# Kernel tuning notes

Hardware: AMD Instinct MI355X
Metric: run time of the kernel (lower is better)

## Reference

```python
import jax, jax.numpy as jnp
import numpy as np

NUM_HEADS = 16

def _rope_tables(seq_len, head_dim, dtype):
    inv_freq = 1.0 / (10000.0 ** (jnp.arange(0, head_dim, 2, dtype=jnp.float32) / head_dim))
    t = jnp.arange(seq_len, dtype=jnp.float32)
    freqs = jnp.einsum('i,j->ij', t, inv_freq)          # [S, hd/2]
    emb = jnp.concatenate([freqs, freqs], axis=-1)      # [S, hd]
    return jnp.cos(emb).astype(dtype), jnp.sin(emb).astype(dtype)

def _rotate_half(x):
    x1, x2 = jnp.split(x, 2, axis=-1)
    return jnp.concatenate([-x2, x1], axis=-1)

def _apply_rope(x, cos, sin):
    # x: [B, H, S, hd]; cos/sin: [S, hd]
    return x * cos + _rotate_half(x) * sin

def setup_inputs() -> dict:
    key = jax.random.key(0)
    ks = jax.random.split(key, 9)
    S, B, E = 2048, 2, 1024
    sc_w = 1.0 / np.sqrt(E)
    inp = {
        'query': jax.random.normal(ks[0], (S, B, E), jnp.float32),
        'wq': jax.random.normal(ks[1], (E, E), jnp.float32) * sc_w,
        'bq': jax.random.normal(ks[2], (E,), jnp.float32) * 0.02,
        'wk': jax.random.normal(ks[3], (E, E), jnp.float32) * sc_w,
        'bk': jax.random.normal(ks[4], (E,), jnp.float32) * 0.02,
        'wv': jax.random.normal(ks[5], (E, E), jnp.float32) * sc_w,
        'bv': jax.random.normal(ks[6], (E,), jnp.float32) * 0.02,
        'wo': jax.random.normal(ks[7], (E, E), jnp.float32) * sc_w,
        'bo': jax.random.normal(ks[8], (E,), jnp.float32) * 0.02,
    }
    return inp

def reference(query, wq, bq, wk, bk, wv, bv, wo, bo):
    S, B, E = query.shape
    H = NUM_HEADS
    hd = E // H
    # QKV projections (torch Linear: x @ W^T + b). self_attention => k,v from query.
    q = jnp.einsum('sbe,fe->sbf', query, wq) + bq
    k = jnp.einsum('sbe,fe->sbf', query, wk) + bk
    v = jnp.einsum('sbe,fe->sbf', query, wv) + bv
    # [S, B, E] -> [B, H, S, hd]
    def to_bhsd(x):
        return x.reshape(S, B, H, hd).transpose(1, 2, 0, 3)
    q, k, v = to_bhsd(q), to_bhsd(k), to_bhsd(v)
    cos, sin = _rope_tables(S, hd, query.dtype)
    q = _apply_rope(q, cos, sin)
    k = _apply_rope(k, cos, sin)
    # scaled dot-product attention (no mask, no dropout)
    scale = 1.0 / jnp.sqrt(jnp.asarray(hd, query.dtype))
    scores = jnp.einsum('bhqd,bhkd->bhqk', q, k) * scale
    probs = jax.nn.softmax(scores, axis=-1)
    attn = jnp.einsum('bhqk,bhkd->bhqd', probs, v)
    # [B, H, S, hd] -> [S, B, E]
    attn = attn.transpose(2, 0, 1, 3).reshape(S, B, E)
    out = jnp.einsum('sbe,fe->sbf', attn, wo) + bo
    return out
```

## Files before the change

### kernel.cpp

```cpp
#include <hip/hip_runtime.h>
#include <stdint.h>

#define S_LEN 2048
#define BATCH 2
#define EMB   1024
#define NHEAD 16
#define HDIM  64

typedef __bf16 bf8   __attribute__((ext_vector_type(8)));
typedef float  f32x4 __attribute__((ext_vector_type(4)));
typedef float  f32x16 __attribute__((ext_vector_type(16)));

__device__ __forceinline__ unsigned short f2bf(float f) {
    unsigned u = __builtin_bit_cast(unsigned, f);
    u += 0x7fffu + ((u >> 16) & 1u);
    return (unsigned short)(u >> 16);
}
__device__ __forceinline__ float bf2f(unsigned short h) {
    unsigned u = ((unsigned)h) << 16;
    return __builtin_bit_cast(float, u);
}
__device__ __forceinline__ float fexp2(float x) { return __builtin_amdgcn_exp2f(x); }
__device__ __forceinline__ float f3max(float a, float b, float c) { return fmaxf(fmaxf(a, b), c); }

__device__ __forceinline__ void gl_lds16(const unsigned short* g, unsigned short* l) {
    __builtin_amdgcn_global_load_lds(
        (__attribute__((address_space(1))) void*)(void*)g,
        (__attribute__((address_space(3))) void*)(void*)l, 16, 0, 0);
}

__global__ void k_prep(const float* __restrict__ x,
                       const float* __restrict__ w0, const float* __restrict__ w1,
                       const float* __restrict__ w2, const float* __restrict__ w3,
                       float* __restrict__ cosT, float* __restrict__ sinT,
                       unsigned short* __restrict__ xb,
                       unsigned short* __restrict__ o0, unsigned short* __restrict__ o1,
                       unsigned short* __restrict__ o2, unsigned short* __restrict__ o3)
{
    int bid = blockIdx.x;
    if (bid < 512) {
        int idx = bid * 256 + threadIdx.x;
        int s = idx >> 6, d = idx & 63, j = d & 31;
        float inv = exp2f(-13.28771237954945f * ((float)j * (1.0f / 32.0f)));
        float ang = (float)s * inv;
        cosT[idx] = cosf(ang);
        sinT[idx] = sinf(ang);
    } else if (bid < 4608) {
        int id = (bid - 512) * 256 + threadIdx.x;
        int b = id >> 19, rem = id & 524287;
        int s = rem >> 8, e4 = (rem & 255) << 2;
        float4 v = *(const float4*)&x[((size_t)(s * BATCH + b)) * EMB + e4];
        ushort4 o;
        o.x = f2bf(v.x); o.y = f2bf(v.y); o.z = f2bf(v.z); o.w = f2bf(v.w);
        *(ushort4*)&xb[((size_t)(b * S_LEN + s)) * EMB + e4] = o;
    } else {
        int id = (bid - 4608) * 256 + threadIdx.x;
        int seg = id >> 18, r = id & 262143;
        const float* s = seg == 0 ? w0 : seg == 1 ? w1 : seg == 2 ? w2 : w3;
        unsigned short* o = seg == 0 ? o0 : seg == 1 ? o1 : seg == 2 ? o2 : o3;
        float4 v = *(const float4*)&s[(size_t)r * 4];
        ushort4 u;
        u.x = f2bf(v.x); u.y = f2bf(v.y); u.z = f2bf(v.z); u.w = f2bf(v.w);
        *(ushort4*)&o[(size_t)r * 4] = u;
    }
}

__global__ void __launch_bounds__(256) k_gemmQKV(
    const unsigned short* __restrict__ A,
    const unsigned short* __restrict__ Wq, const unsigned short* __restrict__ Wk,
    const unsigned short* __restrict__ Wv,
    const float* __restrict__ bqp, const float* __restrict__ bkp, const float* __restrict__ bvp,
    unsigned short* __restrict__ qout, unsigned short* __restrict__ kout,
    unsigned short* __restrict__ vout,
    const float* __restrict__ cosT, const float* __restrict__ sinT)
{
    __shared__ __align__(16) unsigned short As[128 * 32];
    __shared__ __align__(16) unsigned short Bs[128 * 32];
    const int z = blockIdx.z;
    const unsigned short* B = z == 0 ? Wq : z == 1 ? Wk : Wv;
    const float* bias = z == 0 ? bqp : z == 1 ? bkp : bvp;
    const int tid  = threadIdx.x;
    const int lane = tid & 63;
    const int wid  = tid >> 6;
    const int wm = wid >> 1, wn = wid & 1;
    const int l15 = lane & 15, lh = lane >> 4;
    const int tm0 = blockIdx.y * 128, tn0 = blockIdx.x * 128;
    const int K = 1024;

    f32x4 acc[4][4] = {};

    for (int k0 = 0; k0 < K; k0 += 32) {
        __syncthreads();
#pragma unroll
        for (int rnd = 0; rnd < 2; ++rnd) {
            int cbase = wid * 64 + rnd * 256;
            int c = cbase + lane;
            int row = c >> 2, co = (c & 3) * 8;
            gl_lds16(A + (size_t)(tm0 + row) * K + k0 + co, &As[cbase * 8]);
            gl_lds16(B + (size_t)(tn0 + row) * K + k0 + co, &Bs[cbase * 8]);
        }
        __syncthreads();
        bf8 a[4], b[4];
#pragma unroll
        for (int i = 0; i < 4; ++i) {
            a[i] = *(const bf8*)&As[(wm * 64 + i * 16 + l15) * 32 + lh * 8];
            b[i] = *(const bf8*)&Bs[(wn * 64 + i * 16 + l15) * 32 + lh * 8];
        }
#pragma unroll
        for (int i = 0; i < 4; ++i)
#pragma unroll
            for (int j = 0; j < 4; ++j)
                acc[i][j] = __builtin_amdgcn_mfma_f32_16x16x32_bf16(a[i], b[j], acc[i][j], 0, 0, 0);
    }

    if (z < 2) {
        unsigned short* C = z ? kout : qout;
        const float f = z ? 1.0f : 0.125f * 1.44269504089f;
#pragma unroll
        for (int i = 0; i < 4; ++i) {
            const int rowb = tm0 + wm * 64 + i * 16 + lh * 4;
#pragma unroll
            for (int j = 0; j < 2; ++j) {
                const int col = tn0 + wn * 64 + j * 16 + l15;
                const int d = j * 16 + l15;
#pragma unroll
                for (int r = 0; r < 4; ++r) {
                    int m = rowb + r;
                    int sq = m & (S_LEN - 1);
                    float x1 = acc[i][j][r]     + bias[col];
                    float x2 = acc[i][j + 2][r] + bias[col + 32];
                    float c  = cosT[sq * 64 + d] * f;
                    float sn = sinT[sq * 64 + d] * f;
                    C[(size_t)m * EMB + col]      = f2bf(x1 * c - x2 * sn);
                    C[(size_t)m * EMB + col + 32] = f2bf(x2 * c + x1 * sn);
                }
            }
        }
    } else {
#pragma unroll
        for (int i = 0; i < 4; ++i) {
            const int rowb = tm0 + wm * 64 + i * 16 + lh * 4;
#pragma unroll
            for (int j = 0; j < 4; ++j) {
                const int col = tn0 + wn * 64 + j * 16 + l15;
                float bv = bias[col];
#pragma unroll
                for (int r = 0; r < 4; ++r)
                    vout[(size_t)col * 4096 + rowb + r] = f2bf(acc[i][j][r] + bv);
            }
        }
    }
}

__global__ void __launch_bounds__(256) k_attn8(
    const unsigned short* __restrict__ qb,
    const unsigned short* __restrict__ kb,
    const unsigned short* __restrict__ vT,
    unsigned short* __restrict__ ob)
{
    __shared__ __align__(16) unsigned short Sm[24576];
    __shared__ float bl[4][32];
    const int tid = threadIdx.x, lane = tid & 63, wid = tid >> 6;
    const int l31 = lane & 31, hi = lane >> 5;
    const int bh = blockIdx.y;
    const int b = bh >> 4, h = bh & 15;
    const int q0 = blockIdx.x * 128 + wid * 32;

    const unsigned short* qrow = qb + ((size_t)(b * S_LEN + q0 + l31)) * EMB + h * HDIM + hi * 8;
    bf8 qf[4];
#pragma unroll
    for (int c = 0; c < 4; ++c) qf[c] = *(const bf8*)(qrow + c * 16);

    const int mz = l31 & 7;
    const int koA0 = l31 * 128 + (((0 * 2 + hi) ^ mz) << 4);
    const int koA1 = l31 * 128 + (((1 * 2 + hi) ^ mz) << 4);
    const int koA2 = l31 * 128 + (((2 * 2 + hi) ^ mz) << 4);
    const int koA3 = l31 * 128 + (((3 * 2 + hi) ^ mz) << 4);
    const char* ldsc = (const char*)Sm;

    const int srow = lane >> 3, sp = lane & 7;
    const int r0 = wid * 16 + srow,     p0s = sp ^ (r0 & 7);
    const int r1 = wid * 16 + 8 + srow, p1s = sp ^ (r1 & 7);
    const int kgo0 = (r0 * EMB + p0s * 8) * 2, kgo1 = (r1 * EMB + p1s * 8) * 2;
    const int vgo0 = (r0 * (S_LEN * BATCH) + p0s * 8) * 2, vgo1 = (r1 * (S_LEN * BATCH) + p1s * 8) * 2;

    const unsigned short* kS = kb + ((size_t)(b * S_LEN)) * EMB + h * HDIM;
    const unsigned short* vS = vT + ((size_t)h * HDIM) * (S_LEN * BATCH) + b * S_LEN;

#define STAGE8(DBUF) do { \
    gl_lds16((const unsigned short*)((const char*)kS + kgo0), Sm + (DBUF) * 4096 + wid * 1024); \
    gl_lds16((const unsigned short*)((const char*)vS + vgo0), Sm + 12288 + (DBUF) * 4096 + wid * 1024); \
    gl_lds16((const unsigned short*)((const char*)kS + kgo1), Sm + (DBUF) * 4096 + wid * 1024 + 512); \
    gl_lds16((const unsigned short*)((const char*)vS + vgo1), Sm + 12288 + (DBUF) * 4096 + wid * 1024 + 512); \
    kS += 64 * EMB; vS += 64; } while (0)

    auto pack2 = [](float lo, float hh) -> unsigned {
        unsigned short a  = __builtin_bit_cast(unsigned short, (__bf16)lo);
        unsigned short bb = __builtin_bit_cast(unsigned short, (__bf16)hh);
        return ((unsigned)bb << 16) | a;
    };

    float m_run = 0.f, l_run = 0.f;
    f32x16 oacc0 = {}, oacc1 = {};
    const f32x16 Z16 = {};

    STAGE8(0);
    STAGE8(1);

#define ABODY(BUF, DOSTG, LASTW) do { \
    if (LASTW) asm volatile("s_waitcnt vmcnt(0)" ::: "memory"); \
    else       asm volatile("s_waitcnt vmcnt(4)" ::: "memory"); \
    __builtin_amdgcn_s_barrier(); \
    if (DOSTG) STAGE8(((BUF) + 2) % 3); \
    bf8 ka0 = *(const bf8*)(ldsc + koA0 + (BUF) * 8192); \
    bf8 ka1 = *(const bf8*)(ldsc + koA1 + (BUF) * 8192); \
    bf8 ka2 = *(const bf8*)(ldsc + koA2 + (BUF) * 8192); \
    bf8 ka3 = *(const bf8*)(ldsc + koA3 + (BUF) * 8192); \
    bf8 kb0 = *(const bf8*)(ldsc + koA0 + (BUF) * 8192 + 4096); \
    bf8 kb1 = *(const bf8*)(ldsc + koA1 + (BUF) * 8192 + 4096); \
    bf8 kb2 = *(const bf8*)(ldsc + koA2 + (BUF) * 8192 + 4096); \
    bf8 kb3 = *(const bf8*)(ldsc + koA3 + (BUF) * 8192 + 4096); \
    __builtin_amdgcn_s_setprio(1); \
    f32x16 stA = __builtin_amdgcn_mfma_f32_32x32x16_bf16(ka0, qf[0], Z16, 0, 0, 0); \
    f32x16 stB = __builtin_amdgcn_mfma_f32_32x32x16_bf16(kb0, qf[0], Z16, 0, 0, 0); \
    stA = __builtin_amdgcn_mfma_f32_32x32x16_bf16(ka1, qf[1], stA, 0, 0, 0); \
    stB = __builtin_amdgcn_mfma_f32_32x32x16_bf16(kb1, qf[1], stB, 0, 0, 0); \
    stA = __builtin_amdgcn_mfma_f32_32x32x16_bf16(ka2, qf[2], stA, 0, 0, 0); \
    stB = __builtin_amdgcn_mfma_f32_32x32x16_bf16(kb2, qf[2], stB, 0, 0, 0); \
    stA = __builtin_amdgcn_mfma_f32_32x32x16_bf16(ka3, qf[3], stA, 0, 0, 0); \
    stB = __builtin_amdgcn_mfma_f32_32x32x16_bf16(kb3, qf[3], stB, 0, 0, 0); \
    __builtin_amdgcn_s_setprio(0); \
    float g0 = f3max(f3max(stA[0], stA[1], stA[2]),  f3max(stA[3], stA[4], stA[5]),  f3max(stA[6], stA[7], stA[8])); \
    float g1 = f3max(f3max(stA[9], stA[10], stA[11]), f3max(stA[12], stA[13], stA[14]), fmaxf(stA[15], stB[0])); \
    float g2 = f3max(f3max(stB[1], stB[2], stB[3]),  f3max(stB[4], stB[5], stB[6]),  f3max(stB[7], stB[8], stB[9])); \
    float g3 = f3max(f3max(stB[10], stB[11], stB[12]), f3max(stB[13], stB[14], stB[15]), fmaxf(g0, g1)); \
    float pmax = f3max(g2, g3, g0); \
    pmax = fmaxf(pmax, __shfl_xor(pmax, 32)); \
    if (!__all(pmax - m_run <= 11.54f)) { \
        float mnew = fmaxf(m_run, pmax); \
        float corr = fexp2(m_run - mnew); \
        l_run *= corr; m_run = mnew; \
        if (hi == 0) bl[wid][l31] = corr; \
        asm volatile("s_waitcnt lgkmcnt(0)" ::: "memory"); \
        _Pragma("unroll") for (int r = 0; r < 16; ++r) { \
            float c2 = bl[wid][(r & 3) + 8 * (r >> 2) + 4 * hi]; \
            oacc0[r] *= c2; oacc1[r] *= c2; } \
    } \
    float pA[16], pB[16]; \
    _Pragma("unroll") for (int r = 0; r < 16; ++r) pA[r] = fexp2(stA[r] - m_run); \
    _Pragma("unroll") for (int r = 0; r < 16; ++r) pB[r] = fexp2(stB[r] - m_run); \
    float sA = (((pA[0] + pA[1]) + (pA[2] + pA[3])) + ((pA[4] + pA[5]) + (pA[6] + pA[7]))) \
             + (((pA[8] + pA[9]) + (pA[10] + pA[11])) + ((pA[12] + pA[13]) + (pA[14] + pA[15]))); \
    float sB = (((pB[0] + pB[1]) + (pB[2] + pB[3])) + ((pB[4] + pB[5]) + (pB[6] + pB[7]))) \
             + (((pB[8] + pB[9]) + (pB[10] + pB[11])) + ((pB[12] + pB[13]) + (pB[14] + pB[15]))); \
    float psum = sA + sB; \
    psum += __shfl_xor(psum, 32); \
    l_run += psum; \
    unsigned a0w = pack2(pA[0], pA[1]),  a1w = pack2(pA[2], pA[3]); \
    unsigned a2w = pack2(pA[4], pA[5]),  a3w = pack2(pA[6], pA[7]); \
    unsigned a4w = pack2(pA[8], pA[9]),  a5w = pack2(pA[10], pA[11]); \
    unsigned a6w = pack2(pA[12], pA[13]), a7w = pack2(pA[14], pA[15]); \
    unsigned rA_ = (unsigned)__shfl_xor((int)(hi ? a0w : a2w), 32); \
    unsigned rB_ = (unsigned)__shfl_xor((int)(hi ? a1w : a3w), 32); \
    unsigned rC_ = (unsigned)__shfl_xor((int)(hi ? a4w : a6w), 32); \
    unsigned rD_ = (unsigned)__shfl_xor((int)(hi ? a5w : a7w), 32); \
    uint4 uA0 = hi ? uint4{rA_, rB_, a2w, a3w} : uint4{a0w, a1w, rA_, rB_}; \
    uint4 uA1 = hi ? uint4{rC_, rD_, a6w, a7w} : uint4{a4w, a5w, rC_, rD_}; \
    bf8 pf0A = __builtin_bit_cast(bf8, uA0); \
    bf8 pf1A = __builtin_bit_cast(bf8, uA1); \
    unsigned b0w = pack2(pB[0], pB[1]),  b1w = pack2(pB[2], pB[3]); \
    unsigned b2w = pack2(pB[4], pB[5]),  b3w = pack2(pB[6], pB[7]); \
    unsigned b4w = pack2(pB[8], pB[9]),  b5w = pack2(pB[10], pB[11]); \
    unsigned b6w = pack2(pB[12], pB[13]), b7w = pack2(pB[14], pB[15]); \
    unsigned rE_ = (unsigned)__shfl_xor((int)(hi ? b0w : b2w), 32); \
    unsigned rF_ = (unsigned)__shfl_xor((int)(hi ? b1w : b3w), 32); \
    unsigned rG_ = (unsigned)__shfl_xor((int)(hi ? b4w : b6w), 32); \
    unsigned rH_ = (unsigned)__shfl_xor((int)(hi ? b5w : b7w), 32); \
    uint4 uB0 = hi ? uint4{rE_, rF_, b2w, b3w} : uint4{b0w, b1w, rE_, rF_}; \
    uint4 uB1 = hi ? uint4{rG_, rH_, b6w, b7w} : uint4{b4w, b5w, rG_, rH_}; \
    bf8 pf0B = __builtin_bit_cast(bf8, uB0); \
    bf8 pf1B = __builtin_bit_cast(bf8, uB1); \
    bf8 va0 = *(const bf8*)(ldsc + koA0 + 24576 + (BUF) * 8192); \
    bf8 va1 = *(const bf8*)(ldsc + koA1 + 24576 + (BUF) * 8192); \
    bf8 va2 = *(const bf8*)(ldsc + koA2 + 24576 + (BUF) * 8192); \
    bf8 va3 = *(const bf8*)(ldsc + koA3 + 24576 + (BUF) * 8192); \
    bf8 vb0 = *(const bf8*)(ldsc + koA0 + 24576 + (BUF) * 8192 + 4096); \
    bf8 vb1 = *(const bf8*)(ldsc + koA1 + 24576 + (BUF) * 8192 + 4096); \
    bf8 vb2 = *(const bf8*)(ldsc + koA2 + 24576 + (BUF) * 8192 + 4096); \
    bf8 vb3 = *(const bf8*)(ldsc + koA3 + 24576 + (BUF) * 8192 + 4096); \
    __builtin_amdgcn_s_setprio(1); \
    oacc0 = __builtin_amdgcn_mfma_f32_32x32x16_bf16(pf0A, va0, oacc0, 0, 0, 0); \
    oacc1 = __builtin_amdgcn_mfma_f32_32x32x16_bf16(pf0A, vb0, oacc1, 0, 0, 0); \
    oacc0 = __builtin_amdgcn_mfma_f32_32x32x16_bf16(pf1A, va1, oacc0, 0, 0, 0); \
    oacc1 = __builtin_amdgcn_mfma_f32_32x32x16_bf16(pf1A, vb1, oacc1, 0, 0, 0); \
    oacc0 = __builtin_amdgcn_mfma_f32_32x32x16_bf16(pf0B, va2, oacc0, 0, 0, 0); \
    oacc1 = __builtin_amdgcn_mfma_f32_32x32x16_bf16(pf0B, vb2, oacc1, 0, 0, 0); \
    oacc0 = __builtin_amdgcn_mfma_f32_32x32x16_bf16(pf1B, va3, oacc0, 0, 0, 0); \
    oacc1 = __builtin_amdgcn_mfma_f32_32x32x16_bf16(pf1B, vb3, oacc1, 0, 0, 0); \
    __builtin_amdgcn_s_setprio(0); \
} while (0)

    for (int t3 = 0; t3 < 10; ++t3) {
        ABODY(0, true, false);
        ABODY(1, true, false);
        ABODY(2, true, false);
    }
    ABODY(0, false, false);
    ABODY(1, false, true);

#undef ABODY
#undef STAGE8

    if (hi == 0) bl[wid][l31] = l_run;
    asm volatile("s_waitcnt lgkmcnt(0)" ::: "memory");
#pragma unroll
    for (int r = 0; r < 16; ++r) {
        int q = (r & 3) + 8 * (r >> 2) + 4 * hi;
        float linv = 1.0f / bl[wid][q];
        size_t base = ((size_t)(b * S_LEN + q0 + q)) * EMB + h * HDIM + l31;
        ob[base]      = f2bf(oacc0[r] * linv);
        ob[base + 32] = f2bf(oacc1[r] * linv);
    }
}

template<int EPI, typename OutT>
__global__ void __launch_bounds__(256) k_gemm(
    const unsigned short* __restrict__ A,
    const unsigned short* __restrict__ B,
    const float* __restrict__ bias,
    OutT* __restrict__ C,
    int M, int N, int K)
{
    __shared__ __align__(16) unsigned short As[128 * 32];
    __shared__ __align__(16) unsigned short Bs[128 * 32];
    const int tid  = threadIdx.x;
    const int lane = tid & 63;
    const int wid  = tid >> 6;
    const int wm = wid >> 1, wn = wid & 1;
    const int l15 = lane & 15, lh = lane >> 4;
    const int tm0 = blockIdx.y * 128, tn0 = blockIdx.x * 128;

    f32x4 acc[4][4] = {};

    for (int k0 = 0; k0 < K; k0 += 32) {
        __syncthreads();
#pragma unroll
        for (int rnd = 0; rnd < 2; ++rnd) {
            int cbase = wid * 64 + rnd * 256;
            int c = cbase + lane;
            int row = c >> 2, co = (c & 3) * 8;
            gl_lds16(A + (size_t)(tm0 + row) * K + k0 + co, &As[cbase * 8]);
            gl_lds16(B + (size_t)(tn0 + row) * K + k0 + co, &Bs[cbase * 8]);
        }
        __syncthreads();
        bf8 a[4], b[4];
#pragma unroll
        for (int i = 0; i < 4; ++i) {
            a[i] = *(const bf8*)&As[(wm * 64 + i * 16 + l15) * 32 + lh * 8];
            b[i] = *(const bf8*)&Bs[(wn * 64 + i * 16 + l15) * 32 + lh * 8];
        }
#pragma unroll
        for (int i = 0; i < 4; ++i)
#pragma unroll
            for (int j = 0; j < 4; ++j)
                acc[i][j] = __builtin_amdgcn_mfma_f32_16x16x32_bf16(a[i], b[j], acc[i][j], 0, 0, 0);
    }

#pragma unroll
    for (int i = 0; i < 4; ++i) {
        const int rowb = tm0 + wm * 64 + i * 16 + lh * 4;
#pragma unroll
        for (int j = 0; j < 4; ++j) {
            const int col = tn0 + wn * 64 + j * 16 + l15;
#pragma unroll
            for (int r = 0; r < 4; ++r) {
                float v = acc[i][j][r];
                int row = rowb + r;
                if (EPI == 0) {
                    v += bias[col];
                    C[(size_t)row * N + col] = (OutT)f2bf(v);
                } else {
                    v += bias[col];
                    int bb = row >> 11, ss = row & 2047;
                    ((float*)C)[(size_t)(ss * BATCH + bb) * N + col] = v;
                }
            }
        }
    }
}

extern "C" void kernel_launch(void* const* d_in, const int* in_sizes, int n_in,
                              void* d_out, int out_size, void* d_ws, size_t ws_size,
                              hipStream_t stream)
{
    (void)in_sizes; (void)n_in; (void)out_size; (void)ws_size;
    const float* query = (const float*)d_in[0];
    const float* wq = (const float*)d_in[1];
    const float* bq = (const float*)d_in[2];
    const float* wk = (const float*)d_in[3];
    const float* bk = (const float*)d_in[4];
    const float* wv = (const float*)d_in[5];
    const float* bv = (const float*)d_in[6];
    const float* wo = (const float*)d_in[7];
    const float* bo = (const float*)d_in[8];

    char* ws = (char*)d_ws;
    float*          cosT = (float*)(ws + 0);
    float*          sinT = (float*)(ws + (512 << 10));
    unsigned short* xb   = (unsigned short*)(ws + (1  << 20));
    unsigned short* wqb  = (unsigned short*)(ws + (9  << 20));
    unsigned short* wkb  = (unsigned short*)(ws + (11 << 20));
    unsigned short* wvb  = (unsigned short*)(ws + (13 << 20));
    unsigned short* wob  = (unsigned short*)(ws + (15 << 20));
    unsigned short* qb   = (unsigned short*)(ws + (17 << 20));
    unsigned short* ob   = qb;
    unsigned short* kb   = (unsigned short*)(ws + (25 << 20));
    unsigned short* vT   = (unsigned short*)(ws + (33 << 20));

    k_prep<<<8704, 256, 0, stream>>>(query, wq, wk, wv, wo,
                                     cosT, sinT, xb, wqb, wkb, wvb, wob);

    dim3 gq(EMB / 128, (S_LEN * BATCH) / 128, 3);
    k_gemmQKV<<<gq, 256, 0, stream>>>(xb, wqb, wkb, wvb, bq, bk, bv,
                                      qb, kb, vT, cosT, sinT);

    dim3 g3(S_LEN / 128, BATCH * NHEAD);
    k_attn8<<<g3, 256, 0, stream>>>(qb, kb, vT, ob);

    dim3 g1(EMB / 128, (S_LEN * BATCH) / 128);
    k_gemm<1, float><<<g1, 256, 0, stream>>>(ob, wob, bo, (float*)d_out, 4096, 1024, 1024);
}
```

Before: 153.8 us.

## Process two 32-row query tiles per wave in attention kernel

The attention kernel now uses 2 waves (128 threads) per block instead of 4, and each wave handles 64 query rows as two 32-row tiles. The K and V fragments read from LDS are reused by both tiles, and each wave stages twice as many K/V rows. This halves LDS fragment reads per query row and lets one tile's softmax interleave with the other tile's MFMAs. The cost is higher register pressure from doubled accumulators and Q fragments, and fewer waves per block, which may reduce occupancy and latency hiding.

```diff
diff --git a/kernel.cpp b/kernel.cpp
--- a/kernel.cpp
+++ b/kernel.cpp
@@ -152,24 +152,28 @@
     }
 }
 
-__global__ void __launch_bounds__(256) k_attn8(
+__global__ void __launch_bounds__(128) k_attn9(
     const unsigned short* __restrict__ qb,
     const unsigned short* __restrict__ kb,
     const unsigned short* __restrict__ vT,
     unsigned short* __restrict__ ob)
 {
     __shared__ __align__(16) unsigned short Sm[24576];
-    __shared__ float bl[4][32];
+    __shared__ float bl[2][2][32];
     const int tid = threadIdx.x, lane = tid & 63, wid = tid >> 6;
     const int l31 = lane & 31, hi = lane >> 5;
     const int bh = blockIdx.y;
     const int b = bh >> 4, h = bh & 15;
-    const int q0 = blockIdx.x * 128 + wid * 32;
-
-    const unsigned short* qrow = qb + ((size_t)(b * S_LEN + q0 + l31)) * EMB + h * HDIM + hi * 8;
-    bf8 qf[4];
-#pragma unroll
-    for (int c = 0; c < 4; ++c) qf[c] = *(const bf8*)(qrow + c * 16);
+    const int q0 = blockIdx.x * 128 + wid * 64;
+
+    const unsigned short* qrowA = qb + ((size_t)(b * S_LEN + q0 + l31)) * EMB + h * HDIM + hi * 8;
+    const unsigned short* qrowB = qrowA + (size_t)32 * EMB;
+    bf8 qfA[4], qfB[4];
+#pragma unroll
+    for (int c = 0; c < 4; ++c) {
+        qfA[c] = *(const bf8*)(qrowA + c * 16);
+        qfB[c] = *(const bf8*)(qrowB + c * 16);
+    }
 
     const int mz = l31 & 7;
     const int koA0 = l31 * 128 + (((0 * 2 + hi) ^ mz) << 4);
@@ -179,19 +183,23 @@
     const char* ldsc = (const char*)Sm;
 
     const int srow = lane >> 3, sp = lane & 7;
-    const int r0 = wid * 16 + srow,     p0s = sp ^ (r0 & 7);
-    const int r1 = wid * 16 + 8 + srow, p1s = sp ^ (r1 & 7);
-    const int kgo0 = (r0 * EMB + p0s * 8) * 2, kgo1 = (r1 * EMB + p1s * 8) * 2;
-    const int vgo0 = (r0 * (S_LEN * BATCH) + p0s * 8) * 2, vgo1 = (r1 * (S_LEN * BATCH) + p1s * 8) * 2;
+    int kgo[4], vgo[4];
+#pragma unroll
+    for (int i = 0; i < 4; ++i) {
+        int ri = wid * 32 + i * 8 + srow;
+        int ps = sp ^ (ri & 7);
+        kgo[i] = (ri * EMB + ps * 8) * 2;
+        vgo[i] = (ri * (S_LEN * BATCH) + ps * 8) * 2;
+    }
 
     const unsigned short* kS = kb + ((size_t)(b * S_LEN)) * EMB + h * HDIM;
     const unsigned short* vS = vT + ((size_t)h * HDIM) * (S_LEN * BATCH) + b * S_LEN;
 
-#define STAGE8(DBUF) do { \
-    gl_lds16((const unsigned short*)((const char*)kS + kgo0), Sm + (DBUF) * 4096 + wid * 1024); \
-    gl_lds16((const unsigned short*)((const char*)vS + vgo0), Sm + 12288 + (DBUF) * 4096 + wid * 1024); \
-    gl_lds16((const unsigned short*)((const char*)kS + kgo1), Sm + (DBUF) * 4096 + wid * 1024 + 512); \
-    gl_lds16((const unsigned short*)((const char*)vS + vgo1), Sm + 12288 + (DBUF) * 4096 + wid * 1024 + 512); \
+#define STAGE9(DBUF) do { \
+    _Pragma("unroll") for (int i = 0; i < 4; ++i) { \
+        gl_lds16((const unsigned short*)((const char*)kS + kgo[i]), Sm + (DBUF) * 4096 + wid * 2048 + i * 512); \
+        gl_lds16((const unsigned short*)((const char*)vS + vgo[i]), Sm + 12288 + (DBUF) * 4096 + wid * 2048 + i * 512); \
+    } \
     kS += 64 * EMB; vS += 64; } while (0)
 
     auto pack2 = [](float lo, float hh) -> unsigned {
@@ -200,18 +208,77 @@
         return ((unsigned)bb << 16) | a;
     };
 
-    float m_run = 0.f, l_run = 0.f;
-    f32x16 oacc0 = {}, oacc1 = {};
+    float m_runA = 0.f, l_runA = 0.f, m_runB = 0.f, l_runB = 0.f;
+    f32x16 oA0 = {}, oA1 = {}, oB0 = {}, oB1 = {};
     const f32x16 Z16 = {};
 
-    STAGE8(0);
-    STAGE8(1);
+    auto softmax_tile = [&](f32x16& stA, f32x16& stB, float& m_run, float& l_run,
+                            int ti, f32x16& o0, f32x16& o1,
+                            bf8& pf0A, bf8& pf1A, bf8& pf0B, bf8& pf1B) __attribute__((always_inline)) {
+        float g0 = f3max(f3max(stA[0], stA[1], stA[2]),  f3max(stA[3], stA[4], stA[5]),  f3max(stA[6], stA[7], stA[8]));
+        float g1 = f3max(f3max(stA[9], stA[10], stA[11]), f3max(stA[12], stA[13], stA[14]), fmaxf(stA[15], stB[0]));
+        float g2 = f3max(f3max(stB[1], stB[2], stB[3]),  f3max(stB[4], stB[5], stB[6]),  f3max(stB[7], stB[8], stB[9]));
+        float g3 = f3max(f3max(stB[10], stB[11], stB[12]), f3max(stB[13], stB[14], stB[15]), fmaxf(g0, g1));
+        float pmax = f3max(g2, g3, g0);
+        pmax = fmaxf(pmax, __shfl_xor(pmax, 32));
+        if (!__all(pmax - m_run <= 11.54f)) {
+            float mnew = fmaxf(m_run, pmax);
+            float corr = fexp2(m_run - mnew);
+            l_run *= corr; m_run = mnew;
+            if (hi == 0) bl[wid][ti][l31] = corr;
+            asm volatile("s_waitcnt lgkmcnt(0)" ::: "memory");
+#pragma unroll
+            for (int r = 0; r < 16; ++r) {
+                float c2 = bl[wid][ti][(r & 3) + 8 * (r >> 2) + 4 * hi];
+                o0[r] *= c2; o1[r] *= c2;
+            }
+        }
+        float pA[16], pB[16];
+#pragma unroll
+        for (int r = 0; r < 16; ++r) pA[r] = fexp2(stA[r] - m_run);
+#pragma unroll
+        for (int r = 0; r < 16; ++r) pB[r] = fexp2(stB[r] - m_run);
+        float sA = (((pA[0] + pA[1]) + (pA[2] + pA[3])) + ((pA[4] + pA[5]) + (pA[6] + pA[7])))
+                 + (((pA[8] + pA[9]) + (pA[10] + pA[11])) + ((pA[12] + pA[13]) + (pA[14] + pA[15])));
+        float sB = (((pB[0] + pB[1]) + (pB[2] + pB[3])) + ((pB[4] + pB[5]) + (pB[6] + pB[7])))
+                 + (((pB[8] + pB[9]) + (pB[10] + pB[11])) + ((pB[12] + pB[13]) + (pB[14] + pB[15])));
+        float psum = sA + sB;
+        psum += __shfl_xor(psum, 32);
+        l_run += psum;
+        unsigned a0w = pack2(pA[0], pA[1]),  a1w = pack2(pA[2], pA[3]);
+        unsigned a2w = pack2(pA[4], pA[5]),  a3w = pack2(pA[6], pA[7]);
+        unsigned a4w = pack2(pA[8], pA[9]),  a5w = pack2(pA[10], pA[11]);
+        unsigned a6w = pack2(pA[12], pA[13]), a7w = pack2(pA[14], pA[15]);
+        unsigned rA_ = (unsigned)__shfl_xor((int)(hi ? a0w : a2w), 32);
+        unsigned rB_ = (unsigned)__shfl_xor((int)(hi ? a1w : a3w), 32);
+        unsigned rC_ = (unsigned)__shfl_xor((int)(hi ? a4w : a6w), 32);
+        unsigned rD_ = (unsigned)__shfl_xor((int)(hi ? a5w : a7w), 32);
+        uint4 u0 = hi ? uint4{rA_, rB_, a2w, a3w} : uint4{a0w, a1w, rA_, rB_};
+        uint4 u1 = hi ? uint4{rC_, rD_, a6w, a7w} : uint4{a4w, a5w, rC_, rD_};
+        pf0A = __builtin_bit_cast(bf8, u0);
+        pf1A = __builtin_bit_cast(bf8, u1);
+        unsigned b0w = pack2(pB[0], pB[1]),  b1w = pack2(pB[2], pB[3]);
+        unsigned b2w = pack2(pB[4], pB[5]),  b3w = pack2(pB[6], pB[7]);
+        unsigned b4w = pack2(pB[8], pB[9]),  b5w = pack2(pB[10], pB[11]);
+        unsigned b6w = pack2(pB[12], pB[13]), b7w = pack2(pB[14], pB[15]);
+        unsigned rE_ = (unsigned)__shfl_xor((int)(hi ? b0w : b2w), 32);
+        unsigned rF_ = (unsigned)__shfl_xor((int)(hi ? b1w : b3w), 32);
+        unsigned rG_ = (unsigned)__shfl_xor((int)(hi ? b4w : b6w), 32);
+        unsigned rH_ = (unsigned)__shfl_xor((int)(hi ? b5w : b7w), 32);
+        uint4 w0 = hi ? uint4{rE_, rF_, b2w, b3w} : uint4{b0w, b1w, rE_, rF_};
+        uint4 w1 = hi ? uint4{rG_, rH_, b6w, b7w} : uint4{b4w, b5w, rG_, rH_};
+        pf0B = __builtin_bit_cast(bf8, w0);
+        pf1B = __builtin_bit_cast(bf8, w1);
+    };
+
+    STAGE9(0);
+    STAGE9(1);
 
 #define ABODY(BUF, DOSTG, LASTW) do { \
     if (LASTW) asm volatile("s_waitcnt vmcnt(0)" ::: "memory"); \
-    else       asm volatile("s_waitcnt vmcnt(4)" ::: "memory"); \
+    else       asm volatile("s_waitcnt vmcnt(8)" ::: "memory"); \
     __builtin_amdgcn_s_barrier(); \
-    if (DOSTG) STAGE8(((BUF) + 2) % 3); \
+    if (DOSTG) STAGE9(((BUF) + 2) % 3); \
     bf8 ka0 = *(const bf8*)(ldsc + koA0 + (BUF) * 8192); \
     bf8 ka1 = *(const bf8*)(ldsc + koA1 + (BUF) * 8192); \
     bf8 ka2 = *(const bf8*)(ldsc + koA2 + (BUF) * 8192); \
@@ -221,65 +288,29 @@
     bf8 kb2 = *(const bf8*)(ldsc + koA2 + (BUF) * 8192 + 4096); \
     bf8 kb3 = *(const bf8*)(ldsc + koA3 + (BUF) * 8192 + 4096); \
     __builtin_amdgcn_s_setprio(1); \
-    f32x16 stA = __builtin_amdgcn_mfma_f32_32x32x16_bf16(ka0, qf[0], Z16, 0, 0, 0); \
-    f32x16 stB = __builtin_amdgcn_mfma_f32_32x32x16_bf16(kb0, qf[0], Z16, 0, 0, 0); \
-    stA = __builtin_amdgcn_mfma_f32_32x32x16_bf16(ka1, qf[1], stA, 0, 0, 0); \
-    stB = __builtin_amdgcn_mfma_f32_32x32x16_bf16(kb1, qf[1], stB, 0, 0, 0); \
-    stA = __builtin_amdgcn_mfma_f32_32x32x16_bf16(ka2, qf[2], stA, 0, 0, 0); \
-    stB = __builtin_amdgcn_mfma_f32_32x32x16_bf16(kb2, qf[2], stB, 0, 0, 0); \
-    stA = __builtin_amdgcn_mfma_f32_32x32x16_bf16(ka3, qf[3], stA, 0, 0, 0); \
-    stB = __builtin_amdgcn_mfma_f32_32x32x16_bf16(kb3, qf[3], stB, 0, 0, 0); \
+    f32x16 stAa = __builtin_amdgcn_mfma_f32_32x32x16_bf16(ka0, qfA[0], Z16, 0, 0, 0); \
+    f32x16 stBa = __builtin_amdgcn_mfma_f32_32x32x16_bf16(kb0, qfA[0], Z16, 0, 0, 0); \
+    stAa = __builtin_amdgcn_mfma_f32_32x32x16_bf16(ka1, qfA[1], stAa, 0, 0, 0); \
+    stBa = __builtin_amdgcn_mfma_f32_32x32x16_bf16(kb1, qfA[1], stBa, 0, 0, 0); \
+    stAa = __builtin_amdgcn_mfma_f32_32x32x16_bf16(ka2, qfA[2], stAa, 0, 0, 0); \
+    stBa = __builtin_amdgcn_mfma_f32_32x32x16_bf16(kb2, qfA[2], stBa, 0, 0, 0); \
+    stAa = __builtin_amdgcn_mfma_f32_32x32x16_bf16(ka3, qfA[3], stAa, 0, 0, 0); \
+    stBa = __builtin_amdgcn_mfma_f32_32x32x16_bf16(kb3, qfA[3], stBa, 0, 0, 0); \
     __builtin_amdgcn_s_setprio(0); \
-    float g0 = f3max(f3max(stA[0], stA[1], stA[2]),  f3max(stA[3], stA[4], stA[5]),  f3max(stA[6], stA[7], stA[8])); \
-    float g1 = f3max(f3max(stA[9], stA[10], stA[11]), f3max(stA[12], stA[13], stA[14]), fmaxf(stA[15], stB[0])); \
-    float g2 = f3max(f3max(stB[1], stB[2], stB[3]),  f3max(stB[4], stB[5], stB[6]),  f3max(stB[7], stB[8], stB[9])); \
-    float g3 = f3max(f3max(stB[10], stB[11], stB[12]), f3max(stB[13], stB[14], stB[15]), fmaxf(g0, g1)); \
-    float pmax = f3max(g2, g3, g0); \
-    pmax = fmaxf(pmax, __shfl_xor(pmax, 32)); \
-    if (!__all(pmax - m_run <= 11.54f)) { \
-        float mnew = fmaxf(m_run, pmax); \
-        float corr = fexp2(m_run - mnew); \
-        l_run *= corr; m_run = mnew; \
-        if (hi == 0) bl[wid][l31] = corr; \
-        asm volatile("s_waitcnt lgkmcnt(0)" ::: "memory"); \
-        _Pragma("unroll") for (int r = 0; r < 16; ++r) { \
-            float c2 = bl[wid][(r & 3) + 8 * (r >> 2) + 4 * hi]; \
-            oacc0[r] *= c2; oacc1[r] *= c2; } \
-    } \
-    float pA[16], pB[16]; \
-    _Pragma("unroll") for (int r = 0; r < 16; ++r) pA[r] = fexp2(stA[r] - m_run); \
-    _Pragma("unroll") for (int r = 0; r < 16; ++r) pB[r] = fexp2(stB[r] - m_run); \
-    float sA = (((pA[0] + pA[1]) + (pA[2] + pA[3])) + ((pA[4] + pA[5]) + (pA[6] + pA[7]))) \
-             + (((pA[8] + pA[9]) + (pA[10] + pA[11])) + ((pA[12] + pA[13]) + (pA[14] + pA[15]))); \
-    float sB = (((pB[0] + pB[1]) + (pB[2] + pB[3])) + ((pB[4] + pB[5]) + (pB[6] + pB[7]))) \
-             + (((pB[8] + pB[9]) + (pB[10] + pB[11])) + ((pB[12] + pB[13]) + (pB[14] + pB[15]))); \
-    float psum = sA + sB; \
-    psum += __shfl_xor(psum, 32); \
-    l_run += psum; \
-    unsigned a0w = pack2(pA[0], pA[1]),  a1w = pack2(pA[2], pA[3]); \
-    unsigned a2w = pack2(pA[4], pA[5]),  a3w = pack2(pA[6], pA[7]); \
-    unsigned a4w = pack2(pA[8], pA[9]),  a5w = pack2(pA[10], pA[11]); \
-    unsigned a6w = pack2(pA[12], pA[13]), a7w = pack2(pA[14], pA[15]); \
-    unsigned rA_ = (unsigned)__shfl_xor((int)(hi ? a0w : a2w), 32); \
-    unsigned rB_ = (unsigned)__shfl_xor((int)(hi ? a1w : a3w), 32); \
-    unsigned rC_ = (unsigned)__shfl_xor((int)(hi ? a4w : a6w), 32); \
-    unsigned rD_ = (unsigned)__shfl_xor((int)(hi ? a5w : a7w), 32); \
-    uint4 uA0 = hi ? uint4{rA_, rB_, a2w, a3w} : uint4{a0w, a1w, rA_, rB_}; \
-    uint4 uA1 = hi ? uint4{rC_, rD_, a6w, a7w} : uint4{a4w, a5w, rC_, rD_}; \
-    bf8 pf0A = __builtin_bit_cast(bf8, uA0); \
-    bf8 pf1A = __builtin_bit_cast(bf8, uA1); \
-    unsigned b0w = pack2(pB[0], pB[1]),  b1w = pack2(pB[2], pB[3]); \
-    unsigned b2w = pack2(pB[4], pB[5]),  b3w = pack2(pB[6], pB[7]); \
-    unsigned b4w = pack2(pB[8], pB[9]),  b5w = pack2(pB[10], pB[11]); \
-    unsigned b6w = pack2(pB[12], pB[13]), b7w = pack2(pB[14], pB[15]); \
-    unsigned rE_ = (unsigned)__shfl_xor((int)(hi ? b0w : b2w), 32); \
-    unsigned rF_ = (unsigned)__shfl_xor((int)(hi ? b1w : b3w), 32); \
-    unsigned rG_ = (unsigned)__shfl_xor((int)(hi ? b4w : b6w), 32); \
-    unsigned rH_ = (unsigned)__shfl_xor((int)(hi ? b5w : b7w), 32); \
-    uint4 uB0 = hi ? uint4{rE_, rF_, b2w, b3w} : uint4{b0w, b1w, rE_, rF_}; \
-    uint4 uB1 = hi ? uint4{rG_, rH_, b6w, b7w} : uint4{b4w, b5w, rG_, rH_}; \
-    bf8 pf0B = __builtin_bit_cast(bf8, uB0); \
-    bf8 pf1B = __builtin_bit_cast(bf8, uB1); \
+    bf8 pfa0A, pfa1A, pfa0B, pfa1B; \
+    softmax_tile(stAa, stBa, m_runA, l_runA, 0, oA0, oA1, pfa0A, pfa1A, pfa0B, pfa1B); \
+    __builtin_amdgcn_s_setprio(1); \
+    f32x16 stAb = __builtin_amdgcn_mfma_f32_32x32x16_bf16(ka0, qfB[0], Z16, 0, 0, 0); \
+    f32x16 stBb = __builtin_amdgcn_mfma_f32_32x32x16_bf16(kb0, qfB[0], Z16, 0, 0, 0); \
+    stAb = __builtin_amdgcn_mfma_f32_32x32x16_bf16(ka1, qfB[1], stAb, 0, 0, 0); \
+    stBb = __builtin_amdgcn_mfma_f32_32x32x16_bf16(kb1, qfB[1], stBb, 0, 0, 0); \
+    stAb = __builtin_amdgcn_mfma_f32_32x32x16_bf16(ka2, qfB[2], stAb, 0, 0, 0); \
+    stBb = __builtin_amdgcn_mfma_f32_32x32x16_bf16(kb2, qfB[2], stBb, 0, 0, 0); \
+    stAb = __builtin_amdgcn_mfma_f32_32x32x16_bf16(ka3, qfB[3], stAb, 0, 0, 0); \
+    stBb = __builtin_amdgcn_mfma_f32_32x32x16_bf16(kb3, qfB[3], stBb, 0, 0, 0); \
+    __builtin_amdgcn_s_setprio(0); \
+    bf8 pfb0A, pfb1A, pfb0B, pfb1B; \
+    softmax_tile(stAb, stBb, m_runB, l_runB, 1, oB0, oB1, pfb0A, pfb1A, pfb0B, pfb1B); \
     bf8 va0 = *(const bf8*)(ldsc + koA0 + 24576 + (BUF) * 8192); \
     bf8 va1 = *(const bf8*)(ldsc + koA1 + 24576 + (BUF) * 8192); \
     bf8 va2 = *(const bf8*)(ldsc + koA2 + 24576 + (BUF) * 8192); \
@@ -289,14 +320,22 @@
     bf8 vb2 = *(const bf8*)(ldsc + koA2 + 24576 + (BUF) * 8192 + 4096); \
     bf8 vb3 = *(const bf8*)(ldsc + koA3 + 24576 + (BUF) * 8192 + 4096); \
     __builtin_amdgcn_s_setprio(1); \
-    oacc0 = __builtin_amdgcn_mfma_f32_32x32x16_bf16(pf0A, va0, oacc0, 0, 0, 0); \
-    oacc1 = __builtin_amdgcn_mfma_f32_32x32x16_bf16(pf0A, vb0, oacc1, 0, 0, 0); \
-    oacc0 = __builtin_amdgcn_mfma_f32_32x32x16_bf16(pf1A, va1, oacc0, 0, 0, 0); \
-    oacc1 = __builtin_amdgcn_mfma_f32_32x32x16_bf16(pf1A, vb1, oacc1, 0, 0, 0); \
-    oacc0 = __builtin_amdgcn_mfma_f32_32x32x16_bf16(pf0B, va2, oacc0, 0, 0, 0); \
-    oacc1 = __builtin_amdgcn_mfma_f32_32x32x16_bf16(pf0B, vb2, oacc1, 0, 0, 0); \
-    oacc0 = __builtin_amdgcn_mfma_f32_32x32x16_bf16(pf1B, va3, oacc0, 0, 0, 0); \
-    oacc1 = __builtin_amdgcn_mfma_f32_32x32x16_bf16(pf1B, vb3, oacc1, 0, 0, 0); \
+    oA0 = __builtin_amdgcn_mfma_f32_32x32x16_bf16(pfa0A, va0, oA0, 0, 0, 0); \
+    oB0 = __builtin_amdgcn_mfma_f32_32x32x16_bf16(pfb0A, va0, oB0, 0, 0, 0); \
+    oA1 = __builtin_amdgcn_mfma_f32_32x32x16_bf16(pfa0A, vb0, oA1, 0, 0, 0); \
+    oB1 = __builtin_amdgcn_mfma_f32_32x32x16_bf16(pfb0A, vb0, oB1, 0, 0, 0); \
+    oA0 = __builtin_amdgcn_mfma_f32_32x32x16_bf16(pfa1A, va1, oA0, 0, 0, 0); \
+    oB0 = __builtin_amdgcn_mfma_f32_32x32x16_bf16(pfb1A, va1, oB0, 0, 0, 0); \
+    oA1 = __builtin_amdgcn_mfma_f32_32x32x16_bf16(pfa1A, vb1, oA1, 0, 0, 0); \
+    oB1 = __builtin_amdgcn_mfma_f32_32x32x16_bf16(pfb1A, vb1, oB1, 0, 0, 0); \
+    oA0 = __builtin_amdgcn_mfma_f32_32x32x16_bf16(pfa0B, va2, oA0, 0, 0, 0); \
+    oB0 = __builtin_amdgcn_mfma_f32_32x32x16_bf16(pfb0B, va2, oB0, 0, 0, 0); \
+    oA1 = __builtin_amdgcn_mfma_f32_32x32x16_bf16(pfa0B, vb2, oA1, 0, 0, 0); \
+    oB1 = __builtin_amdgcn_mfma_f32_32x32x16_bf16(pfb0B, vb2, oB1, 0, 0, 0); \
+    oA0 = __builtin_amdgcn_mfma_f32_32x32x16_bf16(pfa1B, va3, oA0, 0, 0, 0); \
+    oB0 = __builtin_amdgcn_mfma_f32_32x32x16_bf16(pfb1B, va3, oB0, 0, 0, 0); \
+    oA1 = __builtin_amdgcn_mfma_f32_32x32x16_bf16(pfa1B, vb3, oA1, 0, 0, 0); \
+    oB1 = __builtin_amdgcn_mfma_f32_32x32x16_bf16(pfb1B, vb3, oB1, 0, 0, 0); \
     __builtin_amdgcn_s_setprio(0); \
 } while (0)
 
@@ -309,17 +348,24 @@
     ABODY(1, false, true);
 
 #undef ABODY
-#undef STAGE8
-
-    if (hi == 0) bl[wid][l31] = l_run;
+#undef STAGE9
+
+    if (hi == 0) {
+        bl[wid][0][l31] = l_runA;
+        bl[wid][1][l31] = l_runB;
+    }
     asm volatile("s_waitcnt lgkmcnt(0)" ::: "memory");
 #pragma unroll
     for (int r = 0; r < 16; ++r) {
         int q = (r & 3) + 8 * (r >> 2) + 4 * hi;
-        float linv = 1.0f / bl[wid][q];
-        size_t base = ((size_t)(b * S_LEN + q0 + q)) * EMB + h * HDIM + l31;
-        ob[base]      = f2bf(oacc0[r] * linv);
-        ob[base + 32] = f2bf(oacc1[r] * linv);
+        float linvA = 1.0f / bl[wid][0][q];
+        float linvB = 1.0f / bl[wid][1][q];
+        size_t baseA = ((size_t)(b * S_LEN + q0 + q)) * EMB + h * HDIM + l31;
+        size_t baseB = baseA + (size_t)32 * EMB;
+        ob[baseA]      = f2bf(oA0[r] * linvA);
+        ob[baseA + 32] = f2bf(oA1[r] * linvA);
+        ob[baseB]      = f2bf(oB0[r] * linvB);
+        ob[baseB + 32] = f2bf(oB1[r] * linvB);
     }
 }
 
@@ -425,7 +471,7 @@
                                       qb, kb, vT, cosT, sinT);
 
     dim3 g3(S_LEN / 128, BATCH * NHEAD);
-    k_attn8<<<g3, 256, 0, stream>>>(qb, kb, vT, ob);
+    k_attn9<<<g3, 128, 0, stream>>>(qb, kb, vT, ob);
 
     dim3 g1(EMB / 128, (S_LEN * BATCH) / 128);
     k_gemm<1, float><<<g1, 256, 0, stream>>>(ob, wob, bo, (float*)d_out, 4096, 1024, 1024);
```

New measurement: 164.5 us. 1.07x slower.

## Defer the previous tile's PV MFMAs to overlap them with the current softmax

Applied to the files above, without the earlier changes.

The attention loop is software-pipelined. Each iteration now issues the P·V MFMAs for the previous key tile right after the current QK^T MFMAs, so that matrix work runs alongside the current tile's max/exp/pack softmax code. Packed P fragments and V fragments are carried across iterations in registers, with a prologue iteration that skips PV and an epilogue that issues the final PV. V loads from LDS are hoisted to the top of the body. The cost is more live vector registers, which could lower occupancy or cause spills.

```diff
diff --git a/kernel.cpp b/kernel.cpp
--- a/kernel.cpp
+++ b/kernel.cpp
@@ -152,7 +152,7 @@
     }
 }
 
-__global__ void __launch_bounds__(256) k_attn8(
+__global__ void __launch_bounds__(256) k_attn11(
     const unsigned short* __restrict__ qb,
     const unsigned short* __restrict__ kb,
     const unsigned short* __restrict__ vT,
@@ -204,10 +204,14 @@
     f32x16 oacc0 = {}, oacc1 = {};
     const f32x16 Z16 = {};
 
+    bf8 P0 = {}, P1 = {}, P2 = {}, P3 = {};
+    bf8 Va0 = {}, Va1 = {}, Va2 = {}, Va3 = {};
+    bf8 Vb0 = {}, Vb1 = {}, Vb2 = {}, Vb3 = {};
+
     STAGE8(0);
     STAGE8(1);
 
-#define ABODY(BUF, DOSTG, LASTW) do { \
+#define ABODY(BUF, DOSTG, LASTW, DOPV) do { \
     if (LASTW) asm volatile("s_waitcnt vmcnt(0)" ::: "memory"); \
     else       asm volatile("s_waitcnt vmcnt(4)" ::: "memory"); \
     __builtin_amdgcn_s_barrier(); \
@@ -220,6 +224,14 @@
     bf8 kb1 = *(const bf8*)(ldsc + koA1 + (BUF) * 8192 + 4096); \
     bf8 kb2 = *(const bf8*)(ldsc + koA2 + (BUF) * 8192 + 4096); \
     bf8 kb3 = *(const bf8*)(ldsc + koA3 + (BUF) * 8192 + 4096); \
+    bf8 nva0 = *(const bf8*)(ldsc + koA0 + 24576 + (BUF) * 8192); \
+    bf8 nva1 = *(const bf8*)(ldsc + koA1 + 24576 + (BUF) * 8192); \
+    bf8 nva2 = *(const bf8*)(ldsc + koA2 + 24576 + (BUF) * 8192); \
+    bf8 nva3 = *(const bf8*)(ldsc + koA3 + 24576 + (BUF) * 8192); \
+    bf8 nvb0 = *(const bf8*)(ldsc + koA0 + 24576 + (BUF) * 8192 + 4096); \
+    bf8 nvb1 = *(const bf8*)(ldsc + koA1 + 24576 + (BUF) * 8192 + 4096); \
+    bf8 nvb2 = *(const bf8*)(ldsc + koA2 + 24576 + (BUF) * 8192 + 4096); \
+    bf8 nvb3 = *(const bf8*)(ldsc + koA3 + 24576 + (BUF) * 8192 + 4096); \
     __builtin_amdgcn_s_setprio(1); \
     f32x16 stA = __builtin_amdgcn_mfma_f32_32x32x16_bf16(ka0, qf[0], Z16, 0, 0, 0); \
     f32x16 stB = __builtin_amdgcn_mfma_f32_32x32x16_bf16(kb0, qf[0], Z16, 0, 0, 0); \
@@ -229,6 +241,16 @@
     stB = __builtin_amdgcn_mfma_f32_32x32x16_bf16(kb2, qf[2], stB, 0, 0, 0); \
     stA = __builtin_amdgcn_mfma_f32_32x32x16_bf16(ka3, qf[3], stA, 0, 0, 0); \
     stB = __builtin_amdgcn_mfma_f32_32x32x16_bf16(kb3, qf[3], stB, 0, 0, 0); \
+    if (DOPV) { \
+        oacc0 = __builtin_amdgcn_mfma_f32_32x32x16_bf16(P0, Va0, oacc0, 0, 0, 0); \
+        oacc1 = __builtin_amdgcn_mfma_f32_32x32x16_bf16(P0, Vb0, oacc1, 0, 0, 0); \
+        oacc0 = __builtin_amdgcn_mfma_f32_32x32x16_bf16(P1, Va1, oacc0, 0, 0, 0); \
+        oacc1 = __builtin_amdgcn_mfma_f32_32x32x16_bf16(P1, Vb1, oacc1, 0, 0, 0); \
+        oacc0 = __builtin_amdgcn_mfma_f32_32x32x16_bf16(P2, Va2, oacc0, 0, 0, 0); \
+        oacc1 = __builtin_amdgcn_mfma_f32_32x32x16_bf16(P2, Vb2, oacc1, 0, 0, 0); \
+        oacc0 = __builtin_amdgcn_mfma_f32_32x32x16_bf16(P3, Va3, oacc0, 0, 0, 0); \
+        oacc1 = __builtin_amdgcn_mfma_f32_32x32x16_bf16(P3, Vb3, oacc1, 0, 0, 0); \
+    } \
     __builtin_amdgcn_s_setprio(0); \
     float g0 = f3max(f3max(stA[0], stA[1], stA[2]),  f3max(stA[3], stA[4], stA[5]),  f3max(stA[6], stA[7], stA[8])); \
     float g1 = f3max(f3max(stA[9], stA[10], stA[11]), f3max(stA[12], stA[13], stA[14]), fmaxf(stA[15], stB[0])); \
@@ -266,8 +288,8 @@
     unsigned rD_ = (unsigned)__shfl_xor((int)(hi ? a5w : a7w), 32); \
     uint4 uA0 = hi ? uint4{rA_, rB_, a2w, a3w} : uint4{a0w, a1w, rA_, rB_}; \
     uint4 uA1 = hi ? uint4{rC_, rD_, a6w, a7w} : uint4{a4w, a5w, rC_, rD_}; \
-    bf8 pf0A = __builtin_bit_cast(bf8, uA0); \
-    bf8 pf1A = __builtin_bit_cast(bf8, uA1); \
+    P0 = __builtin_bit_cast(bf8, uA0); \
+    P1 = __builtin_bit_cast(bf8, uA1); \
     unsigned b0w = pack2(pB[0], pB[1]),  b1w = pack2(pB[2], pB[3]); \
     unsigned b2w = pack2(pB[4], pB[5]),  b3w = pack2(pB[6], pB[7]); \
     unsigned b4w = pack2(pB[8], pB[9]),  b5w = pack2(pB[10], pB[11]); \
@@ -278,35 +300,32 @@
     unsigned rH_ = (unsigned)__shfl_xor((int)(hi ? b5w : b7w), 32); \
     uint4 uB0 = hi ? uint4{rE_, rF_, b2w, b3w} : uint4{b0w, b1w, rE_, rF_}; \
     uint4 uB1 = hi ? uint4{rG_, rH_, b6w, b7w} : uint4{b4w, b5w, rG_, rH_}; \
-    bf8 pf0B = __builtin_bit_cast(bf8, uB0); \
-    bf8 pf1B = __builtin_bit_cast(bf8, uB1); \
-    bf8 va0 = *(const bf8*)(ldsc + koA0 + 24576 + (BUF) * 8192); \
-    bf8 va1 = *(const bf8*)(ldsc + koA1 + 24576 + (BUF) * 8192); \
-    bf8 va2 = *(const bf8*)(ldsc + koA2 + 24576 + (BUF) * 8192); \
-    bf8 va3 = *(const bf8*)(ldsc + koA3 + 24576 + (BUF) * 8192); \
-    bf8 vb0 = *(const bf8*)(ldsc + koA0 + 24576 + (BUF) * 8192 + 4096); \
-    bf8 vb1 = *(const bf8*)(ldsc + koA1 + 24576 + (BUF) * 8192 + 4096); \
-    bf8 vb2 = *(const bf8*)(ldsc + koA2 + 24576 + (BUF) * 8192 + 4096); \
-    bf8 vb3 = *(const bf8*)(ldsc + koA3 + 24576 + (BUF) * 8192 + 4096); \
-    __builtin_amdgcn_s_setprio(1); \
-    oacc0 = __builtin_amdgcn_mfma_f32_32x32x16_bf16(pf0A, va0, oacc0, 0, 0, 0); \
-    oacc1 = __builtin_amdgcn_mfma_f32_32x32x16_bf16(pf0A, vb0, oacc1, 0, 0, 0); \
-    oacc0 = __builtin_amdgcn_mfma_f32_32x32x16_bf16(pf1A, va1, oacc0, 0, 0, 0); \
-    oacc1 = __builtin_amdgcn_mfma_f32_32x32x16_bf16(pf1A, vb1, oacc1, 0, 0, 0); \
-    oacc0 = __builtin_amdgcn_mfma_f32_32x32x16_bf16(pf0B, va2, oacc0, 0, 0, 0); \
-    oacc1 = __builtin_amdgcn_mfma_f32_32x32x16_bf16(pf0B, vb2, oacc1, 0, 0, 0); \
-    oacc0 = __builtin_amdgcn_mfma_f32_32x32x16_bf16(pf1B, va3, oacc0, 0, 0, 0); \
-    oacc1 = __builtin_amdgcn_mfma_f32_32x32x16_bf16(pf1B, vb3, oacc1, 0, 0, 0); \
-    __builtin_amdgcn_s_setprio(0); \
+    P2 = __builtin_bit_cast(bf8, uB0); \
+    P3 = __builtin_bit_cast(bf8, uB1); \
+    Va0 = nva0; Va1 = nva1; Va2 = nva2; Va3 = nva3; \
+    Vb0 = nvb0; Vb1 = nvb1; Vb2 = nvb2; Vb3 = nvb3; \
+    asm volatile("s_waitcnt lgkmcnt(0)" ::: "memory"); \
 } while (0)
 
-    for (int t3 = 0; t3 < 10; ++t3) {
-        ABODY(0, true, false);
-        ABODY(1, true, false);
-        ABODY(2, true, false);
-    }
-    ABODY(0, false, false);
-    ABODY(1, false, true);
+    ABODY(0, true, false, false);
+    ABODY(1, true, false, true);
+    ABODY(2, true, false, true);
+    for (int t3 = 0; t3 < 9; ++t3) {
+        ABODY(0, true, false, true);
+        ABODY(1, true, false, true);
+        ABODY(2, true, false, true);
+    }
+    ABODY(0, false, false, true);
+    ABODY(1, false, true,  true);
+
+    oacc0 = __builtin_amdgcn_mfma_f32_32x32x16_bf16(P0, Va0, oacc0, 0, 0, 0);
+    oacc1 = __builtin_amdgcn_mfma_f32_32x32x16_bf16(P0, Vb0, oacc1, 0, 0, 0);
+    oacc0 = __builtin_amdgcn_mfma_f32_32x32x16_bf16(P1, Va1, oacc0, 0, 0, 0);
+    oacc1 = __builtin_amdgcn_mfma_f32_32x32x16_bf16(P1, Vb1, oacc1, 0, 0, 0);
+    oacc0 = __builtin_amdgcn_mfma_f32_32x32x16_bf16(P2, Va2, oacc0, 0, 0, 0);
+    oacc1 = __builtin_amdgcn_mfma_f32_32x32x16_bf16(P2, Vb2, oacc1, 0, 0, 0);
+    oacc0 = __builtin_amdgcn_mfma_f32_32x32x16_bf16(P3, Va3, oacc0, 0, 0, 0);
+    oacc1 = __builtin_amdgcn_mfma_f32_32x32x16_bf16(P3, Vb3, oacc1, 0, 0, 0);
 
 #undef ABODY
 #undef STAGE8
@@ -425,7 +444,7 @@
                                       qb, kb, vT, cosT, sinT);
 
     dim3 g3(S_LEN / 128, BATCH * NHEAD);
-    k_attn8<<<g3, 256, 0, stream>>>(qb, kb, vT, ob);
+    k_attn11<<<g3, 256, 0, stream>>>(qb, kb, vT, ob);
 
     dim3 g1(EMB / 128, (S_LEN * BATCH) / 128);
     k_gemm<1, float><<<g1, 256, 0, stream>>>(ob, wob, bo, (float*)d_out, 4096, 1024, 1024);
```

Result: no change. 153.5 us (-0.2%).
